# Optimization experiments

Measured on AMD Instinct MI355X. Metric: run time of the kernel, lower is better.

The kernel has to match this reference:

```python
import jax, jax.numpy as jnp
import numpy as np

C = 3.0
K = 1.0 / C
SQRT_K = K ** 0.5
GAMMA = 0.1
LAMBDA_STRUCTURE = 5.0
EPS = 1e-7
MIN_NORM = 1e-15
MAX_SQDIST = 50.0

N_NODES = 100000
HID = 64
E_POS = 250000
E_NEG = 250000
E_NONE = E_POS + E_NEG


def _arcosh(x):
    return jnp.log(x + jnp.sqrt(x * x - 1.0))


def hyp_sqdist(x, y):
    # Minkowski inner product: <x,y>_L = sum(x*y) - 2*x0*y0
    mdot = jnp.sum(x * y, axis=-1) - 2.0 * x[..., 0] * y[..., 0]
    theta = jnp.maximum(-mdot / K, 1.0 + EPS)
    return jnp.minimum(K * _arcosh(theta) ** 2, MAX_SQDIST)


def hyp_proj(x):
    # project onto hyperboloid: x0 = sqrt(K + ||x_1:||^2)
    y = x[..., 1:]
    x0 = jnp.sqrt(K + jnp.sum(y * y, axis=-1, keepdims=True))
    return jnp.concatenate([x0, y], axis=-1)


def hyp_expmap0(u):
    x = u[..., 1:]
    xn = jnp.maximum(jnp.sqrt(jnp.sum(x * x, axis=-1, keepdims=True)), MIN_NORM)
    theta = xn / SQRT_K
    res = jnp.concatenate([SQRT_K * jnp.cosh(theta), SQRT_K * jnp.sinh(theta) * x / xn], axis=-1)
    return hyp_proj(res)


def discriminate(z, ei, lin_w, lin_b):
    v = jnp.concatenate([z[ei[0]], z[ei[1]]], axis=-1)  # [E, 2*HID]
    return jax.nn.log_softmax(v @ lin_w.T + lin_b, axis=-1)


def info_net(v, y, w1, b1, w2, b2):
    # MINE-style critic: concat(edge_feature, label) -> Linear -> ReLU -> Linear -> scalar
    h = jnp.concatenate([v, y[:, None]], axis=-1)
    h = jax.nn.relu(h @ w1.T + b1)
    return (h @ w2.T + b2)[:, 0]


def setup_inputs():
    key = jax.random.key(0)
    ks = jax.random.split(key, 16)
    z = jax.random.normal(ks[0], (N_NODES, HID), dtype=jnp.float32)
    lin_w = 0.05 * jax.random.normal(ks[1], (3, 2 * HID), dtype=jnp.float32)
    lin_b = jnp.zeros((3,), dtype=jnp.float32)
    d_info = 2 * (HID + 1)
    info_w1 = 0.02 * jax.random.normal(ks[2], (d_info, d_info + 1), dtype=jnp.float32)
    info_b1 = jnp.zeros((d_info,), dtype=jnp.float32)
    info_w2 = 0.02 * jax.random.normal(ks[3], (1, d_info), dtype=jnp.float32)
    info_b2 = jnp.zeros((1,), dtype=jnp.float32)
    pos_edge_index = jax.random.randint(ks[4], (2, E_POS), 0, N_NODES)
    neg_edge_index = jax.random.randint(ks[5], (2, E_NEG), 0, N_NODES)
    none_edge_index = jax.random.randint(ks[6], (2, E_NONE), 0, N_NODES)
    none_edge_index2 = jax.random.randint(ks[7], (2, E_NONE), 0, N_NODES)
    pos_k = jax.random.randint(ks[8], (E_POS,), 0, N_NODES)
    neg_k = jax.random.randint(ks[9], (E_NEG,), 0, N_NODES)
    perm = jax.random.permutation(ks[10], E_POS + E_NEG + E_NONE)
    return dict(z=z, lin_w=lin_w, lin_b=lin_b, info_w1=info_w1, info_b1=info_b1,
                info_w2=info_w2, info_b2=info_b2, pos_edge_index=pos_edge_index,
                neg_edge_index=neg_edge_index, none_edge_index=none_edge_index,
                none_edge_index2=none_edge_index2, pos_k=pos_k, neg_k=neg_k, perm=perm)


def reference(z, lin_w, lin_b, info_w1, info_b1, info_w2, info_b2,
              pos_edge_index, neg_edge_index, none_edge_index,
              none_edge_index2, pos_k, neg_k, perm):
    # lift z onto the hyperboloid: proj(expmap0(proj_tan0([z0 | z])))
    vals = jnp.concatenate([z[:, :1], z], axis=1)      # [N, HID+1]
    u = vals.at[:, 0].set(0.0)                          # proj_tan0
    x = hyp_proj(hyp_expmap0(u))                        # [N, HID+1]

    # nll discriminator loss (class targets 0 / 1 / 2)
    nll = (jnp.mean(-discriminate(z, pos_edge_index, lin_w, lin_b)[:, 0])
           + jnp.mean(-discriminate(z, neg_edge_index, lin_w, lin_b)[:, 1])
           + jnp.mean(-discriminate(z, none_edge_index, lin_w, lin_b)[:, 2])) / 3.0

    # structured triplet losses on the hyperboloid
    i, j = pos_edge_index[0], pos_edge_index[1]
    l1 = jnp.mean(jnp.maximum(hyp_sqdist(x[i], x[j]) - hyp_sqdist(x[i], x[pos_k]), 0.0))
    i, j = neg_edge_index[0], neg_edge_index[1]
    l2 = jnp.mean(jnp.maximum(hyp_sqdist(x[i], x[neg_k]) - hyp_sqdist(x[i], x[j]), 0.0))

    # mutual-information (MINE) term on hyperbolic embeddings
    idx = jnp.concatenate([pos_edge_index, neg_edge_index, none_edge_index2], axis=1)
    all_y = jnp.concatenate([
        jnp.zeros((pos_edge_index.shape[1],), jnp.float32),
        jnp.ones((neg_edge_index.shape[1],), jnp.float32),
        jnp.full((none_edge_index2.shape[1],), 2.0, jnp.float32)])
    value = jnp.concatenate([x[idx[0]], x[idx[1]]], axis=1)  # [E_all, 2*(HID+1)]
    info_pred = info_net(value, all_y, info_w1, info_b1, info_w2, info_b2)
    info_shuffle = info_net(value, all_y[perm], info_w1, info_b1, info_w2, info_b2)
    l3 = -(jnp.mean(info_pred) - jnp.log(jnp.mean(jnp.exp(info_shuffle))))

    return nll + LAMBDA_STRUCTURE * (l1 + l2) + GAMMA * l3
```

## Files before the change

kernel.cpp:

```cpp
#include <hip/hip_runtime.h>
#include <hip/hip_fp16.h>
#include <math.h>

#define NN    100000
#define EPOS  250000
#define ENEG  250000
#define ENON  500000
#define E3   1000000
#define NLSE  4096

#define NB_INFO   2560
#define NB_STRUCT 1024
#define NB_NLL    512
#define NB_EDGES  (NB_INFO + NB_STRUCT + NB_NLL)

#define ACC_OFF 0
#define LSE_OFF 256
#define X0_OFF  66048
#define ZA_OFF  466176
#define ZB_OFF  2066176
#define WT_OFF  3666176
#define YBF_OFF 3722752
#define YF8_OFF 22922752
#define PT_OFF  29322752
#define QT_OFF  29522752
#define PM_OFF  29722752
#define QM_OFF  42522752

typedef __attribute__((ext_vector_type(8))) short bh8;
typedef __attribute__((ext_vector_type(4))) float f32x4;
typedef __attribute__((ext_vector_type(2))) float f32x2;


__device__ __forceinline__ unsigned short f2bf(float f) {
  unsigned u = __float_as_uint(f);
  unsigned r = (u + 0x7FFFu + ((u >> 16) & 1u)) >> 16;
  return (unsigned short)r;
}

#if __has_builtin(__builtin_amdgcn_cvt_pk_f32_bf8) && __has_builtin(__builtin_amdgcn_cvt_pk_bf8_f32)
#define HAVE_BF8 1
#endif

__device__ __forceinline__ void de4(unsigned v, float* o) {
#ifdef HAVE_BF8
  f32x2 lo = __builtin_amdgcn_cvt_pk_f32_bf8((int)v, false);
  f32x2 hi = __builtin_amdgcn_cvt_pk_f32_bf8((int)v, true);
  o[0] = lo[0]; o[1] = lo[1]; o[2] = hi[0]; o[3] = hi[1];
#else
  o[0] = __half2float(__ushort_as_half((unsigned short)((v & 0xFFu) << 8)));
  o[1] = __half2float(__ushort_as_half((unsigned short)(((v >> 8) & 0xFFu) << 8)));
  o[2] = __half2float(__ushort_as_half((unsigned short)(((v >> 16) & 0xFFu) << 8)));
  o[3] = __half2float(__ushort_as_half((unsigned short)((v >> 24) << 8)));
#endif
}

__device__ __forceinline__ unsigned pk2(float a, float b) {
  a = fminf(fmaxf(a, -57344.f), 57344.f);
  b = fminf(fmaxf(b, -57344.f), 57344.f);
#ifdef HAVE_BF8
  return (unsigned)__builtin_amdgcn_cvt_pk_bf8_f32(a, b, 0, false) & 0xFFFFu;
#else
  unsigned short ha = __half_as_ushort(__float2half(a));
  unsigned short hb = __half_as_ushort(__float2half(b));
  ha = (unsigned short)((ha + 0x7Fu + ((ha >> 8) & 1u)) >> 8);
  hb = (unsigned short)((hb + 0x7Fu + ((hb >> 8) & 1u)) >> 8);
  return (unsigned)ha | ((unsigned)hb << 8);
#endif
}

__device__ __forceinline__ void breduce2(double v0, double v1, double* g0, double* g1,
                                         double* rbuf) {
#pragma unroll
  for (int m = 32; m; m >>= 1) {
    v0 += __shfl_xor(v0, m, 64);
    v1 += __shfl_xor(v1, m, 64);
  }
  int l = threadIdx.x & 63, w = threadIdx.x >> 6;
  if (l == 0) { rbuf[2 * w] = v0; rbuf[2 * w + 1] = v1; }
  __syncthreads();
  if (threadIdx.x == 0) {
    int nw = blockDim.x >> 6;
    double s0 = 0.0, s1 = 0.0;
    for (int i = 0; i < nw; ++i) { s0 += rbuf[2 * i]; s1 += rbuf[2 * i + 1]; }
    atomicAdd(g0, s0);
    atomicAdd(g1, s1);
  }
}

__device__ __forceinline__ void lse_combine(double& m, double& s, double om, double os) {
  double M = fmax(m, om);
  double sn = 0.0;
  if (m > -INFINITY) sn += s * exp(m - M);
  if (om > -INFINITY) sn += os * exp(om - M);
  m = M;
  s = sn;
}

__device__ __forceinline__ void lse_block_reduce(double lm, double ls, double* out_pair,
                                                 double* rbuf) {
#pragma unroll
  for (int d = 32; d; d >>= 1) {
    double om = __shfl_xor(lm, d, 64);
    double os = __shfl_xor(ls, d, 64);
    lse_combine(lm, ls, om, os);
  }
  __syncthreads();
  int l = threadIdx.x & 63, w = threadIdx.x >> 6;
  if (l == 0) { rbuf[2 * w] = lm; rbuf[2 * w + 1] = ls; }
  __syncthreads();
  if (threadIdx.x == 0) {
    int nw = blockDim.x >> 6;
    double M = rbuf[0], S = rbuf[1];
    for (int i = 1; i < nw; ++i) lse_combine(M, S, rbuf[2 * i], rbuf[2 * i + 1]);
    out_pair[0] = M;
    out_pair[1] = S;
  }
}

__global__ __launch_bounds__(256) void k_init(const float* __restrict__ w1,
                                              double* __restrict__ acc,
                                              double* __restrict__ lse,
                                              unsigned short* __restrict__ wt) {
  int gid = blockIdx.x * 256 + threadIdx.x;
  if (gid < NLSE) { lse[2 * gid] = -INFINITY; lse[2 * gid + 1] = 0.0; }
  if (gid < 8) acc[gid] = 0.0;
  for (int u = threadIdx.x; u < 16 * 104; u += 256) {
    int c = 16 * blockIdx.x + u / 104;
    int k = u % 104;
    float val = 0.f;
    if (c < 130) {
      if (k < 64) val = w1[c * 131 + 1 + k];
      else if (k == 64) val = w1[c * 131];
    } else if (c >= 136 && c < 266) {
      int r = c - 136;
      if (k < 64) val = w1[r * 131 + 66 + k];
      else if (k == 64) val = w1[r * 131 + 65];
    }
    wt[(size_t)c * 104 + k] = f2bf(val);
  }
}

__global__ __launch_bounds__(256) void k_preA(
    const float* __restrict__ z, const float* __restrict__ lin_w,
    float* __restrict__ X0, unsigned short* __restrict__ YBF,
    unsigned char* __restrict__ YF8,
    float4* __restrict__ ZA4, float4* __restrict__ ZB4) {
  __shared__ float WL[384];
  for (int u = threadIdx.x; u < 384; u += 256) {
    int rr = u >> 6, d = u & 63;
    WL[u] = (rr < 3) ? lin_w[rr * 128 + d] : lin_w[(rr - 3) * 128 + 64 + d];
  }
  __syncthreads();
  int n = blockIdx.x * 256 + threadIdx.x;
  if (n >= NN) return;
  const float4* zr = (const float4*)(z + (size_t)n * 64);
  const float4* wl4 = (const float4*)WL;
  float4 zc[16];
  float zn2 = 0.f, d0 = 0.f, d1 = 0.f, d2 = 0.f, d3 = 0.f, d4 = 0.f, d5 = 0.f;
#pragma unroll
  for (int c = 0; c < 16; ++c) {
    float4 v = zr[c];
    zc[c] = v;
    zn2 += v.x * v.x + v.y * v.y + v.z * v.z + v.w * v.w;
    float4 w0 = wl4[c];
    float4 w1r = wl4[16 + c];
    float4 w2r = wl4[32 + c];
    float4 w3 = wl4[48 + c];
    float4 w4 = wl4[64 + c];
    float4 w5 = wl4[80 + c];
    d0 += v.x * w0.x + v.y * w0.y + v.z * w0.z + v.w * w0.w;
    d1 += v.x * w1r.x + v.y * w1r.y + v.z * w1r.z + v.w * w1r.w;
    d2 += v.x * w2r.x + v.y * w2r.y + v.z * w2r.z + v.w * w2r.w;
    d3 += v.x * w3.x + v.y * w3.y + v.z * w3.z + v.w * w3.w;
    d4 += v.x * w4.x + v.y * w4.y + v.z * w4.z + v.w * w4.w;
    d5 += v.x * w5.x + v.y * w5.y + v.z * w5.z + v.w * w5.w;
  }
  float zn = fmaxf(sqrtf(zn2), 1e-15f);
  float t = 1.7320508075688772f * zn;
  float e = __expf(t);
  float sh = 0.5f * (e - __frcp_rn(e));
  float fac = (t < 1e-4f) ? (1.f + t * t * 0.16666667f) : (sh / t);
  float yn2 = fac * fac * zn2;
  float x0 = sqrtf(0.33333333333333333f + yn2);
  X0[n] = x0;
  ZA4[n] = make_float4(d0, d1, d2, 0.f);
  ZB4[n] = make_float4(d3, d4, d5, 0.f);
  ushort4* yrow4 = (ushort4*)(YBF + (size_t)n * 96);
#pragma unroll
  for (int c = 0; c < 16; ++c) {
    float4 v = zc[c];
    ushort4 o;
    o.x = f2bf(fac * v.x); o.y = f2bf(fac * v.y);
    o.z = f2bf(fac * v.z); o.w = f2bf(fac * v.w);
    yrow4[c] = o;
  }
  ushort4 xx; xx.x = f2bf(x0); xx.y = 0; xx.z = 0; xx.w = 0;
  yrow4[16] = xx;
  ushort4 zzero; zzero.x = 0; zzero.y = 0; zzero.z = 0; zzero.w = 0;
#pragma unroll
  for (int c = 17; c < 24; ++c) yrow4[c] = zzero;
  unsigned yu[16];
#pragma unroll
  for (int c = 0; c < 16; ++c) {
    float4 v = zc[c];
    yu[c] = pk2(fac * v.x, fac * v.y) | (pk2(fac * v.z, fac * v.w) << 16);
  }
  uint4* y8 = (uint4*)(YF8 + (size_t)n * 64);
  y8[0] = make_uint4(yu[0], yu[1], yu[2], yu[3]);
  y8[1] = make_uint4(yu[4], yu[5], yu[6], yu[7]);
  y8[2] = make_uint4(yu[8], yu[9], yu[10], yu[11]);
  y8[3] = make_uint4(yu[12], yu[13], yu[14], yu[15]);
}

__global__ __launch_bounds__(256) void k_pqgemm(
    const unsigned short* __restrict__ ybf, const unsigned short* __restrict__ wt,
    unsigned char* __restrict__ Pm, unsigned char* __restrict__ Qm,
    unsigned char* __restrict__ PTb, unsigned char* __restrict__ QTb) {
  __shared__ __align__(16) short WTs[28288];
  {
    float4* d = (float4*)WTs;
    const float4* s = (const float4*)wt;
    for (int u = threadIdx.x; u < 3536; u += 256) d[u] = s[u];
  }
  __syncthreads();
  const int l = threadIdx.x & 63;
  const int w = threadIdx.x >> 6;
  const int col = l & 15, kq = l >> 4;
  for (int tile = blockIdx.x * 4 + w; tile < NN / 16; tile += gridDim.x * 4) {
    const int nb = tile * 16;
    const unsigned short* arow = ybf + (size_t)(nb + col) * 96 + kq * 8;
    bh8 a0 = *(const bh8*)(arow);
    bh8 a1 = *(const bh8*)(arow + 32);
    bh8 a2 = *(const bh8*)(arow + 64);
#pragma unroll
    for (int nt = 0; nt < 17; ++nt) {
      const short* wrow = WTs + (nt * 16 + col) * 104 + kq * 8;
      bh8 b0 = *(const bh8*)(wrow);
      bh8 b1 = *(const bh8*)(wrow + 32);
      bh8 b2 = *(const bh8*)(wrow + 64);
      f32x4 acc = {0.f, 0.f, 0.f, 0.f};
      acc = __builtin_amdgcn_mfma_f32_16x16x32_bf16(a0, b0, acc, 0, 0, 0);
      acc = __builtin_amdgcn_mfma_f32_16x16x32_bf16(a1, b1, acc, 0, 0, 0);
      acc = __builtin_amdgcn_mfma_f32_16x16x32_bf16(a2, b2, acc, 0, 0, 0);
      int out = nt * 16 + col;
      bool pmain = out < 128;
      bool ptail = (out == 128) | (out == 129);
      bool qmain = (out >= 136) & (out < 264);
      bool qtail = (out == 264) | (out == 265);
      if (pmain | ptail | qmain | qtail) {
        unsigned pk01 = pk2(acc[0], acc[1]);
        unsigned pk23 = pk2(acc[2], acc[3]);
        unsigned char by[4] = {(unsigned char)(pk01 & 255u), (unsigned char)((pk01 >> 8) & 255u),
                               (unsigned char)(pk23 & 255u), (unsigned char)((pk23 >> 8) & 255u)};
#pragma unroll
        for (int v = 0; v < 4; ++v) {
          size_t node = (size_t)(nb + kq * 4 + v);
          if (pmain) Pm[node * 128 + out] = by[v];
          else if (ptail) PTb[node * 2 + (out - 128)] = by[v];
          else if (qmain) Qm[node * 128 + (out - 136)] = by[v];
          else QTb[node * 2 + (out - 264)] = by[v];
        }
      }
    }
  }
}

__device__ __forceinline__ float hsq(float mdot) {
  float th = fmaxf(-3.f * mdot, 1.f + 1e-7f);
  float ach = __logf(th + sqrtf(th * th - 1.f));
  return fminf(ach * ach * (1.f / 3.f), 50.f);
}

__global__ __launch_bounds__(256) void k_edges(
    const int* __restrict__ p0, const int* __restrict__ p1,
    const int* __restrict__ n0, const int* __restrict__ n1,
    const int* __restrict__ o0, const int* __restrict__ o1,
    const int* __restrict__ q0, const int* __restrict__ q1,
    const int* __restrict__ pk, const int* __restrict__ nk,
    const int* __restrict__ perm,
    const unsigned char* __restrict__ Pm, const unsigned char* __restrict__ Qm,
    const unsigned short* __restrict__ PT, const unsigned short* __restrict__ QT,
    const unsigned char* __restrict__ YF8, const float* __restrict__ X0,
    const float4* __restrict__ ZA4, const float4* __restrict__ ZB4,
    const float* __restrict__ lin_b,
    const float* __restrict__ w1, const float* __restrict__ b1v,
    const float* __restrict__ w2v,
    double* __restrict__ acc, double* __restrict__ lse) {
  __shared__ double rbuf[8];
  __shared__ double rbuf2[8];

  if (blockIdx.x < NB_INFO) {
    const int s8 = threadIdx.x & 7;
    float byr[16], wyr[16], w2r[16];
#pragma unroll
    for (int q = 0; q < 16; ++q) {
      int k = 16 * s8 + q;
      byr[q] = b1v[k];
      wyr[q] = w1[k * 131 + 130];
      w2r[q] = w2v[k];
    }
    const float byt0 = b1v[128], byt1 = b1v[129];
    const float wyt0 = w1[128 * 131 + 130], wyt1 = w1[129 * 131 + 130];
    const float w2t0 = w2v[128], w2t1 = w2v[129];
    int g = (blockIdx.x * 256 + threadIdx.x) >> 3;
    const int gs = (NB_INFO * 256) >> 3;
    float s1f = 0.f, lm = -INFINITY, lsum = 0.f;

    int ypi_c = 0, ysi_c = 0;
    uint4 P_c = {}, Q_c = {};
    unsigned pt_c = 0, qt_c = 0;

#define INFO_FETCH(E, YPI, YSI, P4, Q4, PT_, QT_)                                        \
  {                                                                                      \
    int i, j;                                                                            \
    if ((E) < EPOS) { i = p0[E]; j = p1[E]; YPI = 0; }                                   \
    else if ((E) < EPOS + ENEG) { int t = (E) - EPOS; i = n0[t]; j = n1[t]; YPI = 1; }   \
    else { int t = (E) - EPOS - ENEG; i = q0[t]; j = q1[t]; YPI = 2; }                   \
    int p = perm[E];                                                                     \
    YSI = (p < EPOS) ? 0 : ((p < EPOS + ENEG) ? 1 : 2);                                  \
    P4 = *(const uint4*)(Pm + (size_t)i * 128 + 16 * s8);                                \
    Q4 = *(const uint4*)(Qm + (size_t)j * 128 + 16 * s8);                                \
    if (s8 == 0) { PT_ = PT[i]; QT_ = QT[j]; }                                           \
  }

    int e = g;
    if (e < E3) INFO_FETCH(e, ypi_c, ysi_c, P_c, Q_c, pt_c, qt_c);
    while (e < E3) {
      int e2 = e + gs;
      int ypi_n = 0, ysi_n = 0;
      uint4 P_n = {}, Q_n = {};
      unsigned pt_n = 0, qt_n = 0;
      if (e2 < E3) INFO_FETCH(e2, ypi_n, ysi_n, P_n, Q_n, pt_n, qt_n);

      float pv[16], qv[16];
      de4(P_c.x, pv); de4(P_c.y, pv + 4); de4(P_c.z, pv + 8); de4(P_c.w, pv + 12);
      de4(Q_c.x, qv); de4(Q_c.y, qv + 4); de4(Q_c.z, qv + 8); de4(Q_c.w, qv + 12);
      float ypf = (float)ypi_c, ysf = (float)ysi_c;
      float sp = 0.f, ss = 0.f;
#pragma unroll
      for (int q = 0; q < 16; ++q) {
        float t = pv[q] + qv[q] + byr[q];
        sp = fmaf(fmaxf(fmaf(ypf, wyr[q], t), 0.f), w2r[q], sp);
        ss = fmaf(fmaxf(fmaf(ysf, wyr[q], t), 0.f), w2r[q], ss);
      }
      if (s8 == 0) {
        float tp[4], tq[4];
        de4(pt_c, tp); de4(qt_c, tq);
        float t0 = tp[0] + tq[0] + byt0;
        float t1 = tp[1] + tq[1] + byt1;
        sp += fmaxf(fmaf(ypf, wyt0, t0), 0.f) * w2t0 + fmaxf(fmaf(ypf, wyt1, t1), 0.f) * w2t1;
        ss += fmaxf(fmaf(ysf, wyt0, t0), 0.f) * w2t0 + fmaxf(fmaf(ysf, wyt1, t1), 0.f) * w2t1;
      }
#pragma unroll
      for (int m = 4; m; m >>= 1) {
        sp += __shfl_xor(sp, m, 64);
        ss += __shfl_xor(ss, m, 64);
      }
      if (s8 == 0) {
        s1f += sp;
        float nm = fmaxf(lm, ss);
        lsum = lsum * __expf(lm - nm) + __expf(ss - nm);
        lm = nm;
      }
      e = e2;
      ypi_c = ypi_n; ysi_c = ysi_n; P_c = P_n; Q_c = Q_n; pt_c = pt_n; qt_c = qt_n;
    }
    breduce2((double)s1f, 0.0, acc + 3, acc + 6, rbuf);
    double lmd = (lsum > 0.f) ? (double)lm : -(double)INFINITY;
    lse_block_reduce(lmd, (double)lsum, lse + 2 * blockIdx.x, rbuf2);

  } else if (blockIdx.x < NB_INFO + NB_STRUCT) {
    const int st = threadIdx.x & 7;
    int g = ((blockIdx.x - NB_INFO) * 256 + threadIdx.x) >> 3;
    const int gs = (NB_STRUCT * 256) >> 3;
    float s1f = 0.f, s2f = 0.f;

    bool pos_c = false;
    uint2 yi_c = {}, yj_c = {}, yk_c = {};
    float xi_c = 0.f, xj_c = 0.f, xk_c = 0.f;

#define ST_FETCH(E, POS, YI, YJ, YK, XI, XJ, XK)                       \
  {                                                                    \
    int i, j, kk;                                                      \
    POS = (E) < EPOS;                                                  \
    if (POS) { i = p0[E]; j = p1[E]; kk = pk[E]; }                     \
    else { int t = (E) - EPOS; i = n0[t]; j = n1[t]; kk = nk[t]; }     \
    YI = *(const uint2*)(YF8 + (size_t)i * 64 + 8 * st);               \
    YJ = *(const uint2*)(YF8 + (size_t)j * 64 + 8 * st);               \
    YK = *(const uint2*)(YF8 + (size_t)kk * 64 + 8 * st);              \
    if (st == 0) { XI = X0[i]; XJ = X0[j]; XK = X0[kk]; }              \
  }

    int e = g;
    if (e < EPOS + ENEG) ST_FETCH(e, pos_c, yi_c, yj_c, yk_c, xi_c, xj_c, xk_c);
    while (e < EPOS + ENEG) {
      int e2 = e + gs;
      bool pos_n = false;
      uint2 yi_n = {}, yj_n = {}, yk_n = {};
      float xi_n = 0.f, xj_n = 0.f, xk_n = 0.f;
      if (e2 < EPOS + ENEG) ST_FETCH(e2, pos_n, yi_n, yj_n, yk_n, xi_n, xj_n, xk_n);
      float ai[8], aj[8], ak[8];
      de4(yi_c.x, ai); de4(yi_c.y, ai + 4);
      de4(yj_c.x, aj); de4(yj_c.y, aj + 4);
      de4(yk_c.x, ak); de4(yk_c.y, ak + 4);
      float dij = 0.f, dik = 0.f;
#pragma unroll
      for (int q = 0; q < 8; ++q) {
        dij = fmaf(ai[q], aj[q], dij);
        dik = fmaf(ai[q], ak[q], dik);
      }
#pragma unroll
      for (int m = 4; m; m >>= 1) {
        dij += __shfl_xor(dij, m, 64);
        dik += __shfl_xor(dik, m, 64);
      }
      if (st == 0) {
        float sij = hsq(dij - xi_c * xj_c);
        float sik = hsq(dik - xi_c * xk_c);
        if (pos_c) s1f += fmaxf(sij - sik, 0.f);
        else s2f += fmaxf(sik - sij, 0.f);
      }
      e = e2;
      pos_c = pos_n; yi_c = yi_n; yj_c = yj_n; yk_c = yk_n;
      xi_c = xi_n; xj_c = xj_n; xk_c = xk_n;
    }
    breduce2((double)s1f, (double)s2f, acc + 1, acc + 2, rbuf);

  } else {
    const float c0 = lin_b[0], c1 = lin_b[1], c2 = lin_b[2];
    const float wp = 1.f / (3.f * EPOS), wn = 1.f / (3.f * ENEG), wo = 1.f / (3.f * ENON);
    double s = 0.0;
    int t0 = (blockIdx.x - NB_INFO - NB_STRUCT) * 256 + threadIdx.x;
    for (int e = t0; e < E3; e += NB_NLL * 256) {
      int i, j, tgt;
      float wgt;
      if (e < EPOS) { i = p0[e]; j = p1[e]; tgt = 0; wgt = wp; }
      else if (e < EPOS + ENEG) { int t = e - EPOS; i = n0[t]; j = n1[t]; tgt = 1; wgt = wn; }
      else { int t = e - EPOS - ENEG; i = o0[t]; j = o1[t]; tgt = 2; wgt = wo; }
      float4 a = ZA4[i], b = ZB4[j];
      float l0 = a.x + b.x + c0, l1 = a.y + b.y + c1, l2 = a.z + b.z + c2;
      float mx = fmaxf(l0, fmaxf(l1, l2));
      float lsev = mx + __logf(__expf(l0 - mx) + __expf(l1 - mx) + __expf(l2 - mx));
      float lt = (tgt == 0) ? l0 : ((tgt == 1) ? l1 : l2);
      s += (double)((lsev - lt) * wgt);
    }
    breduce2(s, 0.0, acc + 0, acc + 5, rbuf);
  }
}

__global__ void k_final(const double* __restrict__ acc, const double* __restrict__ lse,
                        float* __restrict__ out) {
  __shared__ double rb[8];
  double lm = -INFINITY, ls = 0.0;
  for (int i = threadIdx.x; i < NLSE; i += blockDim.x)
    lse_combine(lm, ls, lse[2 * i], lse[2 * i + 1]);
#pragma unroll
  for (int d = 32; d; d >>= 1) {
    double om = __shfl_xor(lm, d, 64);
    double os = __shfl_xor(ls, d, 64);
    lse_combine(lm, ls, om, os);
  }
  int l = threadIdx.x & 63, w = threadIdx.x >> 6;
  if (l == 0) { rb[2 * w] = lm; rb[2 * w + 1] = ls; }
  __syncthreads();
  if (threadIdx.x == 0) {
    double M = rb[0], S = rb[1];
    int nw = blockDim.x >> 6;
    for (int i = 1; i < nw; ++i) lse_combine(M, S, rb[2 * i], rb[2 * i + 1]);
    double logmean = M + log(S) - log((double)E3);
    double nll = acc[0];
    double l1 = acc[1] / (double)EPOS;
    double l2 = acc[2] / (double)ENEG;
    double s1m = acc[3] / (double)E3;
    double l3 = -(s1m - logmean);
    out[0] = (float)(nll + 5.0 * (l1 + l2) + 0.1 * l3);
  }
}

extern "C" void kernel_launch(void* const* d_in, const int* in_sizes, int n_in,
                              void* d_out, int out_size, void* d_ws, size_t ws_size,
                              hipStream_t stream) {
  const float* z     = (const float*)d_in[0];
  const float* lin_w = (const float*)d_in[1];
  const float* lin_b = (const float*)d_in[2];
  const float* w1    = (const float*)d_in[3];
  const float* b1v   = (const float*)d_in[4];
  const float* w2v   = (const float*)d_in[5];
  const int* pos  = (const int*)d_in[7];
  const int* neg  = (const int*)d_in[8];
  const int* non  = (const int*)d_in[9];
  const int* non2 = (const int*)d_in[10];
  const int* posk = (const int*)d_in[11];
  const int* negk = (const int*)d_in[12];
  const int* perm = (const int*)d_in[13];

  char* ws = (char*)d_ws;
  double* acc = (double*)(ws + ACC_OFF);
  double* lse = (double*)(ws + LSE_OFF);
  float* X0   = (float*)(ws + X0_OFF);
  float4* ZA4 = (float4*)(ws + ZA_OFF);
  float4* ZB4 = (float4*)(ws + ZB_OFF);
  unsigned short* WT  = (unsigned short*)(ws + WT_OFF);
  unsigned short* YBF = (unsigned short*)(ws + YBF_OFF);
  unsigned char* YF8  = (unsigned char*)(ws + YF8_OFF);
  unsigned char* PTb  = (unsigned char*)(ws + PT_OFF);
  unsigned char* QTb  = (unsigned char*)(ws + QT_OFF);
  unsigned char* PM   = (unsigned char*)(ws + PM_OFF);
  unsigned char* QM   = (unsigned char*)(ws + QM_OFF);

  hipLaunchKernelGGL(k_init, dim3(17), dim3(256), 0, stream, w1, acc, lse, WT);
  hipLaunchKernelGGL(k_preA, dim3((NN + 255) / 256), dim3(256), 0, stream,
                     z, lin_w, X0, YBF, YF8, ZA4, ZB4);
  hipLaunchKernelGGL(k_pqgemm, dim3(512), dim3(256), 0, stream, YBF, WT, PM, QM, PTb, QTb);
  hipLaunchKernelGGL(k_edges, dim3(NB_EDGES), dim3(256), 0, stream,
                     pos, pos + EPOS, neg, neg + ENEG, non, non + ENON,
                     non2, non2 + ENON, posk, negk, perm,
                     PM, QM, (const unsigned short*)PTb, (const unsigned short*)QTb,
                     YF8, X0, ZA4, ZB4, lin_b, w1, b1v, w2v, acc, lse);
  hipLaunchKernelGGL(k_final, dim3(1), dim3(256), 0, stream, acc, lse, (float*)d_out);
}
```

Before: 279.5 us.

## Fuse node precompute with P/Q GEMM via LDS and pair info edges per iteration

```diff
diff --git a/kernel.cpp b/kernel.cpp
--- a/kernel.cpp
+++ b/kernel.cpp
@@ -7,11 +7,12 @@
 #define ENEG  250000
 #define ENON  500000
 #define E3   1000000
+#define EHALF 500000
 #define NLSE  4096
 
-#define NB_INFO   2560
-#define NB_STRUCT 1024
-#define NB_NLL    512
+#define NB_INFO   2816
+#define NB_STRUCT 960
+#define NB_NLL    320
 #define NB_EDGES  (NB_INFO + NB_STRUCT + NB_NLL)
 
 #define ACC_OFF 0
@@ -20,12 +21,11 @@
 #define ZA_OFF  466176
 #define ZB_OFF  2066176
 #define WT_OFF  3666176
-#define YBF_OFF 3722752
-#define YF8_OFF 22922752
-#define PT_OFF  29322752
-#define QT_OFF  29522752
-#define PM_OFF  29722752
-#define QM_OFF  42522752
+#define YF8_OFF 3722752
+#define PT_OFF  10122752
+#define QT_OFF  10322752
+#define PM_OFF  10522752
+#define QM_OFF  23322752
 
 typedef __attribute__((ext_vector_type(8))) short bh8;
 typedef __attribute__((ext_vector_type(4))) float f32x4;
@@ -141,126 +141,110 @@
   }
 }
 
-__global__ __launch_bounds__(256) void k_preA(
+__global__ __launch_bounds__(128) void k_pre(
     const float* __restrict__ z, const float* __restrict__ lin_w,
-    float* __restrict__ X0, unsigned short* __restrict__ YBF,
-    unsigned char* __restrict__ YF8,
-    float4* __restrict__ ZA4, float4* __restrict__ ZB4) {
+    const unsigned short* __restrict__ wt,
+    float* __restrict__ X0, unsigned char* __restrict__ YF8,
+    float4* __restrict__ ZA4, float4* __restrict__ ZB4,
+    unsigned char* __restrict__ Pm, unsigned char* __restrict__ Qm,
+    unsigned char* __restrict__ PTb, unsigned char* __restrict__ QTb) {
   __shared__ float WL[384];
-  for (int u = threadIdx.x; u < 384; u += 256) {
+  __shared__ __align__(16) unsigned short YL[128 * 96];
+  for (int u = threadIdx.x; u < 384; u += 128) {
     int rr = u >> 6, d = u & 63;
     WL[u] = (rr < 3) ? lin_w[rr * 128 + d] : lin_w[(rr - 3) * 128 + 64 + d];
   }
   __syncthreads();
-  int n = blockIdx.x * 256 + threadIdx.x;
-  if (n >= NN) return;
-  const float4* zr = (const float4*)(z + (size_t)n * 64);
-  const float4* wl4 = (const float4*)WL;
-  float4 zc[16];
-  float zn2 = 0.f, d0 = 0.f, d1 = 0.f, d2 = 0.f, d3 = 0.f, d4 = 0.f, d5 = 0.f;
-#pragma unroll
-  for (int c = 0; c < 16; ++c) {
-    float4 v = zr[c];
-    zc[c] = v;
-    zn2 += v.x * v.x + v.y * v.y + v.z * v.z + v.w * v.w;
-    float4 w0 = wl4[c];
-    float4 w1r = wl4[16 + c];
-    float4 w2r = wl4[32 + c];
-    float4 w3 = wl4[48 + c];
-    float4 w4 = wl4[64 + c];
-    float4 w5 = wl4[80 + c];
-    d0 += v.x * w0.x + v.y * w0.y + v.z * w0.z + v.w * w0.w;
-    d1 += v.x * w1r.x + v.y * w1r.y + v.z * w1r.z + v.w * w1r.w;
-    d2 += v.x * w2r.x + v.y * w2r.y + v.z * w2r.z + v.w * w2r.w;
-    d3 += v.x * w3.x + v.y * w3.y + v.z * w3.z + v.w * w3.w;
-    d4 += v.x * w4.x + v.y * w4.y + v.z * w4.z + v.w * w4.w;
-    d5 += v.x * w5.x + v.y * w5.y + v.z * w5.z + v.w * w5.w;
-  }
-  float zn = fmaxf(sqrtf(zn2), 1e-15f);
-  float t = 1.7320508075688772f * zn;
-  float e = __expf(t);
-  float sh = 0.5f * (e - __frcp_rn(e));
-  float fac = (t < 1e-4f) ? (1.f + t * t * 0.16666667f) : (sh / t);
-  float yn2 = fac * fac * zn2;
-  float x0 = sqrtf(0.33333333333333333f + yn2);
-  X0[n] = x0;
-  ZA4[n] = make_float4(d0, d1, d2, 0.f);
-  ZB4[n] = make_float4(d3, d4, d5, 0.f);
-  ushort4* yrow4 = (ushort4*)(YBF + (size_t)n * 96);
-#pragma unroll
-  for (int c = 0; c < 16; ++c) {
-    float4 v = zc[c];
-    ushort4 o;
-    o.x = f2bf(fac * v.x); o.y = f2bf(fac * v.y);
-    o.z = f2bf(fac * v.z); o.w = f2bf(fac * v.w);
-    yrow4[c] = o;
-  }
-  ushort4 xx; xx.x = f2bf(x0); xx.y = 0; xx.z = 0; xx.w = 0;
-  yrow4[16] = xx;
-  ushort4 zzero; zzero.x = 0; zzero.y = 0; zzero.z = 0; zzero.w = 0;
-#pragma unroll
-  for (int c = 17; c < 24; ++c) yrow4[c] = zzero;
-  unsigned yu[16];
-#pragma unroll
-  for (int c = 0; c < 16; ++c) {
-    float4 v = zc[c];
-    yu[c] = pk2(fac * v.x, fac * v.y) | (pk2(fac * v.z, fac * v.w) << 16);
-  }
-  uint4* y8 = (uint4*)(YF8 + (size_t)n * 64);
-  y8[0] = make_uint4(yu[0], yu[1], yu[2], yu[3]);
-  y8[1] = make_uint4(yu[4], yu[5], yu[6], yu[7]);
-  y8[2] = make_uint4(yu[8], yu[9], yu[10], yu[11]);
-  y8[3] = make_uint4(yu[12], yu[13], yu[14], yu[15]);
-}
-
-__global__ __launch_bounds__(256) void k_pqgemm(
-    const unsigned short* __restrict__ ybf, const unsigned short* __restrict__ wt,
-    unsigned char* __restrict__ Pm, unsigned char* __restrict__ Qm,
-    unsigned char* __restrict__ PTb, unsigned char* __restrict__ QTb) {
-  __shared__ __align__(16) short WTs[28288];
-  {
-    float4* d = (float4*)WTs;
-    const float4* s = (const float4*)wt;
-    for (int u = threadIdx.x; u < 3536; u += 256) d[u] = s[u];
+  const int base = blockIdx.x * 128;
+  const int n = base + threadIdx.x;
+  if (n < NN) {
+    const float4* zr = (const float4*)(z + (size_t)n * 64);
+    const float4* wl4 = (const float4*)WL;
+    float4 zc[16];
+    float zn2 = 0.f, d0 = 0.f, d1 = 0.f, d2 = 0.f, d3 = 0.f, d4 = 0.f, d5 = 0.f;
+#pragma unroll
+    for (int c = 0; c < 16; ++c) {
+      float4 v = zr[c];
+      zc[c] = v;
+      zn2 += v.x * v.x + v.y * v.y + v.z * v.z + v.w * v.w;
+      float4 w0 = wl4[c];
+      float4 w1r = wl4[16 + c];
+      float4 w2r = wl4[32 + c];
+      float4 w3 = wl4[48 + c];
+      float4 w4 = wl4[64 + c];
+      float4 w5 = wl4[80 + c];
+      d0 += v.x * w0.x + v.y * w0.y + v.z * w0.z + v.w * w0.w;
+      d1 += v.x * w1r.x + v.y * w1r.y + v.z * w1r.z + v.w * w1r.w;
+      d2 += v.x * w2r.x + v.y * w2r.y + v.z * w2r.z + v.w * w2r.w;
+      d3 += v.x * w3.x + v.y * w3.y + v.z * w3.z + v.w * w3.w;
+      d4 += v.x * w4.x + v.y * w4.y + v.z * w4.z + v.w * w4.w;
+      d5 += v.x * w5.x + v.y * w5.y + v.z * w5.z + v.w * w5.w;
+    }
+    float zn = fmaxf(sqrtf(zn2), 1e-15f);
+    float t = 1.7320508075688772f * zn;
+    float e = __expf(t);
+    float sh = 0.5f * (e - __frcp_rn(e));
+    float fac = (t < 1e-4f) ? (1.f + t * t * 0.16666667f) : (sh / t);
+    float yn2 = fac * fac * zn2;
+    float x0 = sqrtf(0.33333333333333333f + yn2);
+    X0[n] = x0;
+    ZA4[n] = make_float4(d0, d1, d2, 0.f);
+    ZB4[n] = make_float4(d3, d4, d5, 0.f);
+    unsigned short* yrow = YL + threadIdx.x * 96;
+    unsigned yu[16];
+#pragma unroll
+    for (int c = 0; c < 16; ++c) {
+      float4 v = zc[c];
+      ushort4 o;
+      o.x = f2bf(fac * v.x); o.y = f2bf(fac * v.y);
+      o.z = f2bf(fac * v.z); o.w = f2bf(fac * v.w);
+      *(ushort4*)(yrow + 4 * c) = o;
+      yu[c] = pk2(fac * v.x, fac * v.y) | (pk2(fac * v.z, fac * v.w) << 16);
+    }
+    ushort4 xx; xx.x = f2bf(x0); xx.y = 0; xx.z = 0; xx.w = 0;
+    *(ushort4*)(yrow + 64) = xx;
+    ushort4 zz; zz.x = 0; zz.y = 0; zz.z = 0; zz.w = 0;
+#pragma unroll
+    for (int c = 17; c < 24; ++c) *(ushort4*)(yrow + 4 * c) = zz;
+    uint4* y8 = (uint4*)(YF8 + (size_t)n * 64);
+    y8[0] = make_uint4(yu[0], yu[1], yu[2], yu[3]);
+    y8[1] = make_uint4(yu[4], yu[5], yu[6], yu[7]);
+    y8[2] = make_uint4(yu[8], yu[9], yu[10], yu[11]);
+    y8[3] = make_uint4(yu[12], yu[13], yu[14], yu[15]);
   }
   __syncthreads();
   const int l = threadIdx.x & 63;
   const int w = threadIdx.x >> 6;
   const int col = l & 15, kq = l >> 4;
-  for (int tile = blockIdx.x * 4 + w; tile < NN / 16; tile += gridDim.x * 4) {
-    const int nb = tile * 16;
-    const unsigned short* arow = ybf + (size_t)(nb + col) * 96 + kq * 8;
-    bh8 a0 = *(const bh8*)(arow);
-    bh8 a1 = *(const bh8*)(arow + 32);
-    bh8 a2 = *(const bh8*)(arow + 64);
+  const int ntiles = min(8, (NN - base) >> 4);
+  for (int t = w; t < ntiles; t += 2) {
+    const unsigned short* yr = YL + (t * 16 + col) * 96 + kq * 8;
+    bh8 y0 = *(const bh8*)(yr);
+    bh8 y1 = *(const bh8*)(yr + 32);
+    bh8 y2 = *(const bh8*)(yr + 64);
+    const size_t node = (size_t)(base + t * 16 + col);
 #pragma unroll
     for (int nt = 0; nt < 17; ++nt) {
-      const short* wrow = WTs + (nt * 16 + col) * 104 + kq * 8;
-      bh8 b0 = *(const bh8*)(wrow);
-      bh8 b1 = *(const bh8*)(wrow + 32);
-      bh8 b2 = *(const bh8*)(wrow + 64);
-      f32x4 acc = {0.f, 0.f, 0.f, 0.f};
-      acc = __builtin_amdgcn_mfma_f32_16x16x32_bf16(a0, b0, acc, 0, 0, 0);
-      acc = __builtin_amdgcn_mfma_f32_16x16x32_bf16(a1, b1, acc, 0, 0, 0);
-      acc = __builtin_amdgcn_mfma_f32_16x16x32_bf16(a2, b2, acc, 0, 0, 0);
-      int out = nt * 16 + col;
-      bool pmain = out < 128;
-      bool ptail = (out == 128) | (out == 129);
-      bool qmain = (out >= 136) & (out < 264);
-      bool qtail = (out == 264) | (out == 265);
-      if (pmain | ptail | qmain | qtail) {
-        unsigned pk01 = pk2(acc[0], acc[1]);
-        unsigned pk23 = pk2(acc[2], acc[3]);
-        unsigned char by[4] = {(unsigned char)(pk01 & 255u), (unsigned char)((pk01 >> 8) & 255u),
-                               (unsigned char)(pk23 & 255u), (unsigned char)((pk23 >> 8) & 255u)};
-#pragma unroll
-        for (int v = 0; v < 4; ++v) {
-          size_t node = (size_t)(nb + kq * 4 + v);
-          if (pmain) Pm[node * 128 + out] = by[v];
-          else if (ptail) PTb[node * 2 + (out - 128)] = by[v];
-          else if (qmain) Qm[node * 128 + (out - 136)] = by[v];
-          else QTb[node * 2 + (out - 264)] = by[v];
-        }
+      const unsigned short* wr = wt + (size_t)(nt * 16 + col) * 104 + kq * 8;
+      bh8 b0 = *(const bh8*)(wr);
+      bh8 b1 = *(const bh8*)(wr + 32);
+      bh8 b2 = *(const bh8*)(wr + 64);
+      f32x4 a4 = {0.f, 0.f, 0.f, 0.f};
+      a4 = __builtin_amdgcn_mfma_f32_16x16x32_bf16(b0, y0, a4, 0, 0, 0);
+      a4 = __builtin_amdgcn_mfma_f32_16x16x32_bf16(b1, y1, a4, 0, 0, 0);
+      a4 = __builtin_amdgcn_mfma_f32_16x16x32_bf16(b2, y2, a4, 0, 0, 0);
+      int ob = nt * 16 + kq * 4;
+      unsigned u = pk2(a4[0], a4[1]) | (pk2(a4[2], a4[3]) << 16);
+      if (nt < 8) {
+        *(unsigned*)(Pm + node * 128 + ob) = u;
+      } else if (nt == 8) {
+        if (kq == 0) *(unsigned short*)(PTb + node * 2) = (unsigned short)pk2(a4[0], a4[1]);
+        else if (kq >= 2) *(unsigned*)(Qm + node * 128 + (ob - 136)) = u;
+      } else if (nt < 16) {
+        *(unsigned*)(Qm + node * 128 + (ob - 136)) = u;
+      } else {
+        if (kq < 2) *(unsigned*)(Qm + node * 128 + (ob - 136)) = u;
+        else if (kq == 2) *(unsigned short*)(QTb + node * 2) = (unsigned short)pk2(a4[0], a4[1]);
       }
     }
   }
@@ -307,64 +291,81 @@
     const int gs = (NB_INFO * 256) >> 3;
     float s1f = 0.f, lm = -INFINITY, lsum = 0.f;
 
-    int ypi_c = 0, ysi_c = 0;
-    uint4 P_c = {}, Q_c = {};
-    unsigned pt_c = 0, qt_c = 0;
-
-#define INFO_FETCH(E, YPI, YSI, P4, Q4, PT_, QT_)                                        \
-  {                                                                                      \
-    int i, j;                                                                            \
-    if ((E) < EPOS) { i = p0[E]; j = p1[E]; YPI = 0; }                                   \
-    else if ((E) < EPOS + ENEG) { int t = (E) - EPOS; i = n0[t]; j = n1[t]; YPI = 1; }   \
-    else { int t = (E) - EPOS - ENEG; i = q0[t]; j = q1[t]; YPI = 2; }                   \
-    int p = perm[E];                                                                     \
-    YSI = (p < EPOS) ? 0 : ((p < EPOS + ENEG) ? 1 : 2);                                  \
-    P4 = *(const uint4*)(Pm + (size_t)i * 128 + 16 * s8);                                \
-    Q4 = *(const uint4*)(Qm + (size_t)j * 128 + 16 * s8);                                \
-    if (s8 == 0) { PT_ = PT[i]; QT_ = QT[j]; }                                           \
+    int yAp_c = 0, yAs_c = 0, yBs_c = 0;
+    uint4 PA_c = {}, QA_c = {}, PB_c = {}, QB_c = {};
+    unsigned ptA_c = 0, qtA_c = 0, ptB_c = 0, qtB_c = 0;
+
+#define FETCH_A(E, YPI, YSI, P4, Q4, PT_, QT_)                                          \
+  {                                                                                     \
+    int i, j;                                                                           \
+    if ((E) < EPOS) { i = p0[E]; j = p1[E]; YPI = 0; }                                  \
+    else { int t_ = (E) - EPOS; i = n0[t_]; j = n1[t_]; YPI = 1; }                      \
+    int p_ = perm[E];                                                                   \
+    YSI = (p_ < EPOS) ? 0 : ((p_ < EPOS + ENEG) ? 1 : 2);                               \
+    P4 = *(const uint4*)(Pm + (size_t)i * 128 + 16 * s8);                               \
+    Q4 = *(const uint4*)(Qm + (size_t)j * 128 + 16 * s8);                               \
+    if (s8 == 0) { PT_ = PT[i]; QT_ = QT[j]; }                                          \
+  }
+#define FETCH_B(E, YSI, P4, Q4, PT_, QT_)                                               \
+  {                                                                                     \
+    int i = q0[E], j = q1[E];                                                           \
+    int p_ = perm[(E) + EHALF];                                                         \
+    YSI = (p_ < EPOS) ? 0 : ((p_ < EPOS + ENEG) ? 1 : 2);                               \
+    P4 = *(const uint4*)(Pm + (size_t)i * 128 + 16 * s8);                               \
+    Q4 = *(const uint4*)(Qm + (size_t)j * 128 + 16 * s8);                               \
+    if (s8 == 0) { PT_ = PT[i]; QT_ = QT[j]; }                                          \
+  }
+#define INFO_COMPUTE(YPF, YSF, P4, Q4, PT_, QT_)                                        \
+  {                                                                                     \
+    float pv[16], qv[16];                                                               \
+    de4(P4.x, pv); de4(P4.y, pv + 4); de4(P4.z, pv + 8); de4(P4.w, pv + 12);            \
+    de4(Q4.x, qv); de4(Q4.y, qv + 4); de4(Q4.z, qv + 8); de4(Q4.w, qv + 12);            \
+    float sp = 0.f, ss = 0.f;                                                           \
+    _Pragma("unroll") for (int q = 0; q < 16; ++q) {                                    \
+      float t_ = pv[q] + qv[q] + byr[q];                                                \
+      sp = fmaf(fmaxf(fmaf(YPF, wyr[q], t_), 0.f), w2r[q], sp);                         \
+      ss = fmaf(fmaxf(fmaf(YSF, wyr[q], t_), 0.f), w2r[q], ss);                         \
+    }                                                                                   \
+    if (s8 == 0) {                                                                      \
+      float tp[4], tq[4];                                                               \
+      de4(PT_, tp); de4(QT_, tq);                                                       \
+      float t0 = tp[0] + tq[0] + byt0;                                                  \
+      float t1 = tp[1] + tq[1] + byt1;                                                  \
+      sp += fmaxf(fmaf(YPF, wyt0, t0), 0.f) * w2t0 + fmaxf(fmaf(YPF, wyt1, t1), 0.f) * w2t1; \
+      ss += fmaxf(fmaf(YSF, wyt0, t0), 0.f) * w2t0 + fmaxf(fmaf(YSF, wyt1, t1), 0.f) * w2t1; \
+    }                                                                                   \
+    _Pragma("unroll") for (int m_ = 4; m_; m_ >>= 1) {                                  \
+      sp += __shfl_xor(sp, m_, 64);                                                     \
+      ss += __shfl_xor(ss, m_, 64);                                                     \
+    }                                                                                   \
+    if (s8 == 0) {                                                                      \
+      s1f += sp;                                                                        \
+      float nm = fmaxf(lm, ss);                                                         \
+      lsum = lsum * __expf(lm - nm) + __expf(ss - nm);                                  \
+      lm = nm;                                                                          \
+    }                                                                                   \
   }
 
     int e = g;
-    if (e < E3) INFO_FETCH(e, ypi_c, ysi_c, P_c, Q_c, pt_c, qt_c);
-    while (e < E3) {
+    if (e < EHALF) {
+      FETCH_A(e, yAp_c, yAs_c, PA_c, QA_c, ptA_c, qtA_c);
+      FETCH_B(e, yBs_c, PB_c, QB_c, ptB_c, qtB_c);
+    }
+    while (e < EHALF) {
       int e2 = e + gs;
-      int ypi_n = 0, ysi_n = 0;
-      uint4 P_n = {}, Q_n = {};
-      unsigned pt_n = 0, qt_n = 0;
-      if (e2 < E3) INFO_FETCH(e2, ypi_n, ysi_n, P_n, Q_n, pt_n, qt_n);
-
-      float pv[16], qv[16];
-      de4(P_c.x, pv); de4(P_c.y, pv + 4); de4(P_c.z, pv + 8); de4(P_c.w, pv + 12);
-      de4(Q_c.x, qv); de4(Q_c.y, qv + 4); de4(Q_c.z, qv + 8); de4(Q_c.w, qv + 12);
-      float ypf = (float)ypi_c, ysf = (float)ysi_c;
-      float sp = 0.f, ss = 0.f;
-#pragma unroll
-      for (int q = 0; q < 16; ++q) {
-        float t = pv[q] + qv[q] + byr[q];
-        sp = fmaf(fmaxf(fmaf(ypf, wyr[q], t), 0.f), w2r[q], sp);
-        ss = fmaf(fmaxf(fmaf(ysf, wyr[q], t), 0.f), w2r[q], ss);
+      int yAp_n = 0, yAs_n = 0, yBs_n = 0;
+      uint4 PA_n = {}, QA_n = {}, PB_n = {}, QB_n = {};
+      unsigned ptA_n = 0, qtA_n = 0, ptB_n = 0, qtB_n = 0;
+      if (e2 < EHALF) {
+        FETCH_A(e2, yAp_n, yAs_n, PA_n, QA_n, ptA_n, qtA_n);
+        FETCH_B(e2, yBs_n, PB_n, QB_n, ptB_n, qtB_n);
       }
-      if (s8 == 0) {
-        float tp[4], tq[4];
-        de4(pt_c, tp); de4(qt_c, tq);
-        float t0 = tp[0] + tq[0] + byt0;
-        float t1 = tp[1] + tq[1] + byt1;
-        sp += fmaxf(fmaf(ypf, wyt0, t0), 0.f) * w2t0 + fmaxf(fmaf(ypf, wyt1, t1), 0.f) * w2t1;
-        ss += fmaxf(fmaf(ysf, wyt0, t0), 0.f) * w2t0 + fmaxf(fmaf(ysf, wyt1, t1), 0.f) * w2t1;
-      }
-#pragma unroll
-      for (int m = 4; m; m >>= 1) {
-        sp += __shfl_xor(sp, m, 64);
-        ss += __shfl_xor(ss, m, 64);
-      }
-      if (s8 == 0) {
-        s1f += sp;
-        float nm = fmaxf(lm, ss);
-        lsum = lsum * __expf(lm - nm) + __expf(ss - nm);
-        lm = nm;
-      }
+      INFO_COMPUTE((float)yAp_c, (float)yAs_c, PA_c, QA_c, ptA_c, qtA_c);
+      INFO_COMPUTE(2.f, (float)yBs_c, PB_c, QB_c, ptB_c, qtB_c);
       e = e2;
-      ypi_c = ypi_n; ysi_c = ysi_n; P_c = P_n; Q_c = Q_n; pt_c = pt_n; qt_c = qt_n;
+      yAp_c = yAp_n; yAs_c = yAs_n; yBs_c = yBs_n;
+      PA_c = PA_n; QA_c = QA_n; PB_c = PB_n; QB_c = QB_n;
+      ptA_c = ptA_n; qtA_c = qtA_n; ptB_c = ptB_n; qtB_c = qtB_n;
     }
     breduce2((double)s1f, 0.0, acc + 3, acc + 6, rbuf);
     double lmd = (lsum > 0.f) ? (double)lm : -(double)INFINITY;
@@ -502,7 +503,6 @@
   float4* ZA4 = (float4*)(ws + ZA_OFF);
   float4* ZB4 = (float4*)(ws + ZB_OFF);
   unsigned short* WT  = (unsigned short*)(ws + WT_OFF);
-  unsigned short* YBF = (unsigned short*)(ws + YBF_OFF);
   unsigned char* YF8  = (unsigned char*)(ws + YF8_OFF);
   unsigned char* PTb  = (unsigned char*)(ws + PT_OFF);
   unsigned char* QTb  = (unsigned char*)(ws + QT_OFF);
@@ -510,9 +510,8 @@
   unsigned char* QM   = (unsigned char*)(ws + QM_OFF);
 
   hipLaunchKernelGGL(k_init, dim3(17), dim3(256), 0, stream, w1, acc, lse, WT);
-  hipLaunchKernelGGL(k_preA, dim3((NN + 255) / 256), dim3(256), 0, stream,
-                     z, lin_w, X0, YBF, YF8, ZA4, ZB4);
-  hipLaunchKernelGGL(k_pqgemm, dim3(512), dim3(256), 0, stream, YBF, WT, PM, QM, PTb, QTb);
+  hipLaunchKernelGGL(k_pre, dim3((NN + 127) / 128), dim3(128), 0, stream,
+                     z, lin_w, WT, X0, YF8, ZA4, ZB4, PM, QM, PTb, QTb);
   hipLaunchKernelGGL(k_edges, dim3(NB_EDGES), dim3(256), 0, stream,
                      pos, pos + EPOS, neg, neg + ENEG, non, non + ENON,
                      non2, non2 + ENON, posk, negk, perm,
```

New measurement: 280.6 us. About the same (+0.4%).
